# Kernel optimization log

Measured on AMD Instinct MI355X. Metric: run time of the kernel, lower is better.

## Reference

```python
import jax, jax.numpy as jnp
import numpy as np

B = 4096
DETER = 2048
BLOCKS = 8
HIDDEN = 256
SC, SD = 32, 16
STOCH = SC * SD  # 512
ACT = 17
EMBED = 1024
UNIMIX = 0.01
EPS = 1e-4
DPB = DETER // BLOCKS  # 256


def rmsnorm(x, scale):
    rms = jnp.sqrt(jnp.mean(x * x, axis=-1, keepdims=True) + EPS)
    return x / rms * scale


def dense(x, w, b):
    return x @ w + b


def block_linear(x, kernel, bias):
    # kernel: (out_per_block, in_per_block, blocks)
    bs = x.shape[:-1]
    ipb = x.shape[-1] // BLOCKS
    xg = x.reshape(*bs, BLOCKS, ipb)
    y = jnp.einsum('...gi,oig->...go', xg, kernel)
    return y.reshape(*bs, -1) + bias


def sample(logits):
    # unimix + straight-through argmax
    probs = jax.nn.softmax(logits, axis=-1)
    probs = (1.0 - UNIMIX) * probs + UNIMIX / SD
    logits = jnp.log(probs + 1e-8)
    soft = jax.nn.softmax(logits, axis=-1)
    hard = jax.nn.one_hot(jnp.argmax(logits, axis=-1), SD, dtype=soft.dtype)
    return hard + soft - jax.lax.stop_gradient(soft)


def setup_inputs() -> dict:
    key = jax.random.key(0)
    ks = jax.random.split(key, 16)

    def lecun(k, shape, fan_in):
        return jax.random.normal(k, shape, jnp.float32) / np.sqrt(fan_in)

    return {
        'stoch': jax.random.uniform(ks[0], (B, SC, SD), jnp.float32),
        'deter': jax.random.normal(ks[1], (B, DETER), jnp.float32),
        'action': jax.random.normal(ks[2], (B, ACT), jnp.float32),
        'embed': jax.random.normal(ks[3], (B, EMBED), jnp.float32),
        # Deter net params
        'in0_w': lecun(ks[4], (DETER, HIDDEN), DETER), 'in0_b': jnp.zeros((HIDDEN,)), 'in_norm0_s': jnp.ones((HIDDEN,)),
        'in1_w': lecun(ks[5], (STOCH, HIDDEN), STOCH), 'in1_b': jnp.zeros((HIDDEN,)), 'in_norm1_s': jnp.ones((HIDDEN,)),
        'in2_w': lecun(ks[6], (ACT, HIDDEN), ACT), 'in2_b': jnp.zeros((HIDDEN,)), 'in_norm2_s': jnp.ones((HIDDEN,)),
        'hid0_k': lecun(ks[7], (DPB, DPB + 3 * HIDDEN, BLOCKS), DPB + 3 * HIDDEN),
        'hid0_b': jnp.zeros((DETER,)), 'hid_norm0_s': jnp.ones((DETER,)),
        'gru_k': lecun(ks[8], (3 * DPB, DPB, BLOCKS), DPB), 'gru_b': jnp.zeros((3 * DETER,)),
        # posterior head
        'obs_fc0_w': lecun(ks[9], (DETER + EMBED, HIDDEN), DETER + EMBED), 'obs_fc0_b': jnp.zeros((HIDDEN,)),
        'obs_norm0_s': jnp.ones((HIDDEN,)),
        'obs_out_w': lecun(ks[10], (HIDDEN, STOCH), HIDDEN), 'obs_out_b': jnp.zeros((STOCH,)),
    }


def reference(stoch, deter, action, embed,
              in0_w, in0_b, in_norm0_s, in1_w, in1_b, in_norm1_s,
              in2_w, in2_b, in_norm2_s, hid0_k, hid0_b, hid_norm0_s,
              gru_k, gru_b, obs_fc0_w, obs_fc0_b, obs_norm0_s,
              obs_out_w, obs_out_b):
    Bn = stoch.shape[0]
    stoch_flat = stoch.reshape(Bn, -1)  # (B, 512)
    act = action / jnp.maximum(jnp.abs(action), 1.0)
    x0 = jax.nn.silu(rmsnorm(dense(deter, in0_w, in0_b), in_norm0_s))
    x1 = jax.nn.silu(rmsnorm(dense(stoch_flat, in1_w, in1_b), in_norm1_s))
    x2 = jax.nn.silu(rmsnorm(dense(act, in2_w, in2_b), in_norm2_s))
    x = jnp.concatenate([x0, x1, x2], axis=-1)  # (B, 768)
    x = jnp.broadcast_to(x[:, None, :], (Bn, BLOCKS, x.shape[-1]))
    deter_blocked = deter.reshape(Bn, BLOCKS, DPB)
    x = jnp.concatenate([deter_blocked, x], axis=-1).reshape(Bn, -1)  # (B, 8192)
    x = jax.nn.silu(rmsnorm(block_linear(x, hid0_k, hid0_b), hid_norm0_s))  # (B, 2048)
    gates = block_linear(x, gru_k, gru_b)  # (B, 6144)
    gates = gates.reshape(Bn, BLOCKS, 3 * DPB)
    g0, g1, g2 = jnp.split(gates, 3, axis=-1)
    reset = jax.nn.sigmoid(g0.reshape(Bn, -1))
    cand = g1.reshape(Bn, -1)
    update = jax.nn.sigmoid(g2.reshape(Bn, -1) - 1.0)
    new_deter = update * jnp.tanh(reset * cand) + (1.0 - update) * deter
    # posterior head
    h = jnp.concatenate([new_deter, embed], axis=-1)
    h = jax.nn.silu(rmsnorm(dense(h, obs_fc0_w, obs_fc0_b), obs_norm0_s))
    logit = dense(h, obs_out_w, obs_out_b).reshape(Bn, SC, SD)
    new_stoch = sample(logit)
    return (new_stoch, new_deter, logit)
```

## Files before the change

### kernel.cpp

```cpp
#include <hip/hip_runtime.h>
#include <cmath>

constexpr int BATCH = 4096;
constexpr float EPSN = 1e-4f;

constexpr int OFF_STOCH = 0;
constexpr int OFF_DETER = BATCH * 512;
constexpr int OFF_LOGIT = OFF_DETER + BATCH * 2048;

typedef unsigned short ushort;
typedef __attribute__((ext_vector_type(4))) float f32x4;
typedef __attribute__((ext_vector_type(8))) short s16x8;
struct us4 { ushort x, y, z, w; };

constexpr size_t U_WHH = 0;
constexpr size_t U_WHL = U_WHH + 2097152;
constexpr size_t U_WGH = U_WHL + 2097152;
constexpr size_t U_WGL = U_WGH + 1572864;
constexpr size_t U_WFH = U_WGL + 1572864;
constexpr size_t U_WFL = U_WFH + 786432;
constexpr size_t U_WOH = U_WFL + 786432;
constexpr size_t U_WOL = U_WOH + 131072;
constexpr size_t U_PEND = U_WOL + 131072;
constexpr size_t F_XB = U_PEND / 2;
constexpr size_t F_XH = F_XB + 3145728;
constexpr size_t U_X0H = (F_XH + 6291456) * 2;
constexpr size_t U_X0L = U_X0H + 524288;
constexpr size_t U_X1H = U_X0L + 524288;
constexpr size_t U_X1L = U_X1H + 131072;
constexpr size_t F_HB = F_XH + 4194304;

#define DINLINE __device__ __forceinline__

DINLINE float sigm(float x)  { return 1.0f / (1.0f + expf(-x)); }
DINLINE float siluf(float x) { return x / (1.0f + expf(-x)); }

DINLINE float4 ld4(const float* p) { return *reinterpret_cast<const float4*>(p); }
DINLINE void st4(float* p, float4 v) { *reinterpret_cast<float4*>(p) = v; }

DINLINE ushort f2bf(float x) {
  unsigned u = __float_as_uint(x);
  unsigned r = u + 0x7fffu + ((u >> 16) & 1u);
  return (ushort)(r >> 16);
}
DINLINE float bf2f(ushort h) { return __uint_as_float(((unsigned)h) << 16); }

DINLINE void cp16g(void* lds, const void* g) {
  __builtin_amdgcn_global_load_lds(
      (const __attribute__((address_space(1))) unsigned int*)g,
      (__attribute__((address_space(3))) unsigned int*)lds, 16, 0, 0);
}

DINLINE f32x4 mfma16(s16x8 a, s16x8 b, f32x4 c) {
  return __builtin_amdgcn_mfma_f32_16x16x32_bf16(a, b, c, 0, 0, 0);
}

DINLINE int swz_addr(int row, int kb0) {
  return (row * 64 + kb0) ^ ((row & 7) << 4);
}
DINLINE void dec_swz(int D, int& row, int& kb) {
  int r2 = (D >> 8) & 1;
  int r0 = ((D >> 6) & 1) ^ r2;
  row = ((D >> 7) << 1) | r0;
  kb = (D & 48) ^ ((row & 3) << 4);
}

DINLINE void split2(float x, ushort& h, ushort& l) {
  h = f2bf(x);
  l = f2bf(x - bf2f(h));
}

DINLINE size_t frag_idx(int n, int k, int NK) {
  return ((size_t)((n >> 4) * NK + (k >> 5)) * 64 + ((k >> 3) & 3) * 16 + (n & 15)) * 8 + (k & 7);
}

DINLINE float4 rms_silu4(float v0, float v1, float v2, float v3, float4 s4) {
  float ss = v0 * v0 + v1 * v1 + v2 * v2 + v3 * v3;
#pragma unroll
  for (int off = 32; off; off >>= 1) ss += __shfl_xor(ss, off);
  float inv = 1.0f / sqrtf(ss * (1.0f / 256.0f) + EPSN);
  float4 o;
  o.x = siluf(v0 * inv * s4.x); o.y = siluf(v1 * inv * s4.y);
  o.z = siluf(v2 * inv * s4.z); o.w = siluf(v3 * inv * s4.w);
  return o;
}

__global__ __launch_bounds__(256) void k_prep(
    const float* __restrict__ hk, const float* __restrict__ gk,
    const float* __restrict__ w0, const float* __restrict__ w1,
    const float* __restrict__ wf, const float* __restrict__ wo,
    ushort* __restrict__ wsU) {
  __shared__ float L[64 * 65];
  const int bid = blockIdx.x, tid = threadIdx.x;
  if (bid < 1792) {
    int t = bid * 256 + tid;
    if (t < 262144) {
      int o = t >> 10, i = t & 1023;
      const float* src = hk + (size_t)t * 8;
      float4 v0 = ld4(src), v1 = ld4(src + 4);
      float vv[8] = {v0.x, v0.y, v0.z, v0.w, v1.x, v1.y, v1.z, v1.w};
      size_t fi = frag_idx(o, i, 32);
#pragma unroll
      for (int g2 = 0; g2 < 8; ++g2) {
        ushort h, l; split2(vv[g2], h, l);
        wsU[U_WHH + (size_t)g2 * 262144 + fi] = h;
        wsU[U_WHL + (size_t)g2 * 262144 + fi] = l;
      }
    } else {
      int e = t - 262144;
      int o = e >> 8, i = e & 255;
      const float* src = gk + (size_t)e * 8;
      float4 v0 = ld4(src), v1 = ld4(src + 4);
      float vv[8] = {v0.x, v0.y, v0.z, v0.w, v1.x, v1.y, v1.z, v1.w};
      int gate = o >> 8, nc = (o >> 6) & 3, srow = gate * 64 + (o & 63);
      size_t fi = frag_idx(srow, i, 8);
#pragma unroll
      for (int g2 = 0; g2 < 8; ++g2) {
        ushort h, l; split2(vv[g2], h, l);
        size_t pb = (size_t)(g2 * 4 + nc) * 49152;
        wsU[U_WGH + pb + fi] = h;
        wsU[U_WGL + pb + fi] = l;
      }
    }
    return;
  }
  int t = bid - 1792;
  const float* src; ushort* dh; ushort* dl; int K, N;
  if (t < 128)      { src = w0; dh = wsU + U_X0H; dl = wsU + U_X0L; K = 2048; N = 256; }
  else if (t < 160) { t -= 128; src = w1; dh = wsU + U_X1H; dl = wsU + U_X1L; K = 512;  N = 256; }
  else if (t < 352) { t -= 160; src = wf; dh = wsU + U_WFH; dl = wsU + U_WFL; K = 3072; N = 256; }
  else              { t -= 352; src = wo; dh = wsU + U_WOH; dl = wsU + U_WOL; K = 256;  N = 512; }
  const int NK = K / 32;
  const int ntiles = N / 64;
  const int k0 = (t / ntiles) * 64, n0 = (t % ntiles) * 64;
#pragma unroll
  for (int q = 0; q < 4; ++q) {
    int row = q * 16 + (tid >> 4), col = (tid & 15) * 4;
    float4 v = ld4(src + (size_t)(k0 + row) * N + n0 + col);
    L[row * 65 + col]     = v.x;
    L[row * 65 + col + 1] = v.y;
    L[row * 65 + col + 2] = v.z;
    L[row * 65 + col + 3] = v.w;
  }
  __syncthreads();
  const int nl = tid >> 2, kc = (tid & 3) * 16;
  const int ng = n0 + nl;
  s16x8 h0, h1, l0v, l1v;
#pragma unroll
  for (int j = 0; j < 16; ++j) {
    ushort h, l; split2(L[(kc + j) * 65 + nl], h, l);
    if (j < 8) { h0[j] = (short)h; l0v[j] = (short)l; }
    else       { h1[j - 8] = (short)h; l1v[j - 8] = (short)l; }
  }
  size_t fa = frag_idx(ng, k0 + kc, NK);
  size_t fb = frag_idx(ng, k0 + kc + 8, NK);
  *(s16x8*)(dh + fa) = h0;
  *(s16x8*)(dh + fb) = h1;
  *(s16x8*)(dl + fa) = l0v;
  *(s16x8*)(dl + fb) = l1v;
}

__global__ __launch_bounds__(512) void k_gemm256(
    int mode,
    const float* __restrict__ deter, const float* __restrict__ stoch,
    const float* __restrict__ newdet, const float* __restrict__ embed,
    const ushort* __restrict__ wsU, float* __restrict__ part) {
  __shared__ ushort Ah[2][64 * 32], Al[2][64 * 32];
  const int tid = threadIdx.x, lane = tid & 63, wv = tid >> 6;
  const int wr = wv >> 2, wc = wv & 3;
  const int bid = blockIdx.x;
  constexpr size_t PL0 = (size_t)4096 * 512;

  const float* A0; const float* A1 = nullptr;
  int lda0, lda1 = 0, ksw = 1 << 30;
  const ushort* wFh; const ushort* wFl;
  int NKt, kch0, kbase, KT, m0, dstride, dcol;
  float* dst;

  if (mode == 0) {
    if (bid < 256) {
      int ks = bid & 3; m0 = (bid >> 2) * 64; kbase = ks * 512; KT = 16;
      A0 = deter; lda0 = 2048;
      wFh = wsU + U_X0H; wFl = wsU + U_X0L; NKt = 64; kch0 = ks * 16;
      dst = part + (size_t)(ks >> 1) * PL0; dstride = 512; dcol = (ks & 1) * 256;
    } else {
      int b = bid - 256; int ks = b & 1; m0 = (b >> 1) * 64; kbase = ks * 256; KT = 8;
      A0 = stoch; lda0 = 512;
      wFh = wsU + U_X1H; wFl = wsU + U_X1L; NKt = 16; kch0 = ks * 8;
      dst = part + 2 * PL0; dstride = 512; dcol = ks * 256;
    }
  } else {
    int ks = bid & 3; m0 = (bid >> 2) * 64; kbase = ks * 768; KT = 24;
    A0 = newdet; lda0 = 2048; A1 = embed; lda1 = 1024; ksw = 2048;
    wFh = wsU + U_WFH; wFl = wsU + U_WFL; NKt = 96; kch0 = ks * 24;
    dst = part + (size_t)ks * 4096 * 256; dstride = 256; dcol = 0;
  }

  const int arow = tid >> 2, akq = (tid & 3) * 8;
  const int abyte = swz_addr(arow, (tid & 3) * 16);
  float av[8];

  const f32x4 z4 = {0.f, 0.f, 0.f, 0.f};
  f32x4 acc[2][4];
#pragma unroll
  for (int i = 0; i < 2; ++i)
#pragma unroll
    for (int j = 0; j < 4; ++j) acc[i][j] = z4;

#define U_LOADA(kt) \
  if (tid < 256) { \
    int kg = kbase + (kt) * 32 + akq; \
    const float* p = (kg < ksw) ? A0 + (size_t)(m0 + arow) * lda0 + kg \
                                : A1 + (size_t)(m0 + arow) * lda1 + (kg - ksw); \
    float4 u_ = ld4(p), w_ = ld4(p + 4); \
    av[0] = u_.x; av[1] = u_.y; av[2] = u_.z; av[3] = u_.w; \
    av[4] = w_.x; av[5] = w_.y; av[6] = w_.z; av[7] = w_.w; \
  }
#define U_WRITEA(buf) \
  if (tid < 256) { \
    s16x8 h8, l8; \
    _Pragma("unroll") \
    for (int j = 0; j < 8; ++j) { \
      ushort h_, l_; split2(av[j], h_, l_); \
      h8[j] = (short)h_; l8[j] = (short)l_; \
    } \
    *(s16x8*)((char*)Ah[buf] + abyte) = h8; \
    *(s16x8*)((char*)Al[buf] + abyte) = l8; \
  }

  U_LOADA(0);
  U_WRITEA(0);
  __syncthreads();
  int cur = 0;
  for (int t = 0; t < KT; ++t) {
    if (t + 1 < KT) { U_LOADA(t + 1); }
    s16x8 bh[4], bl[4];
#pragma unroll
    for (int nf = 0; nf < 4; ++nf) {
      size_t fo = ((size_t)((wc * 4 + nf) * NKt + kch0 + t) * 64 + lane) * 8;
      bh[nf] = *(const s16x8*)(wFh + fo);
      bl[nf] = *(const s16x8*)(wFl + fo);
    }
    const int k16 = (lane >> 4) * 16;
    s16x8 afh[2], afl[2];
#pragma unroll
    for (int mf = 0; mf < 2; ++mf) {
      int by = swz_addr(wr * 32 + mf * 16 + (lane & 15), k16);
      afh[mf] = *(const s16x8*)((const char*)Ah[cur] + by);
      afl[mf] = *(const s16x8*)((const char*)Al[cur] + by);
    }
#pragma unroll
    for (int nf = 0; nf < 4; ++nf) {
#pragma unroll
      for (int mf = 0; mf < 2; ++mf) {
        acc[mf][nf] = mfma16(afh[mf], bh[nf], acc[mf][nf]);
        acc[mf][nf] = mfma16(afh[mf], bl[nf], acc[mf][nf]);
        acc[mf][nf] = mfma16(afl[mf], bh[nf], acc[mf][nf]);
      }
    }
    if (t + 1 < KT) { U_WRITEA(cur ^ 1); }
    __syncthreads();
    cur ^= 1;
  }
#undef U_LOADA
#undef U_WRITEA
#pragma unroll
  for (int mf = 0; mf < 2; ++mf) {
    int rbase = m0 + wr * 32 + mf * 16 + ((lane >> 4) << 2);
#pragma unroll
    for (int nf = 0; nf < 4; ++nf) {
      int col = dcol + wc * 64 + nf * 16 + (lane & 15);
#pragma unroll
      for (int r = 0; r < 4; ++r)
        dst[(size_t)(rbase + r) * dstride + col] = acc[mf][nf][r];
    }
  }
}

__global__ __launch_bounds__(512) void k_x2(
    const float* __restrict__ action, const float* __restrict__ w2,
    const float* __restrict__ b2, const float* __restrict__ s2,
    ushort* __restrict__ xbp) {
  __shared__ float W2s[17 * 256];
  __shared__ float A2s[128 * 20];
  const int tid = threadIdx.x, tx = tid & 63, wv = tid >> 6;
  const int m0 = blockIdx.x * 128;
  for (int e = tid; e < 17 * 256; e += 512) W2s[e] = w2[e];
  for (int e = tid; e < 128 * 17; e += 512) {
    int r = e / 17, c = e % 17;
    float a = action[(size_t)(m0 + r) * 17 + c];
    float m = fabsf(a);
    A2s[r * 20 + c] = a / (m > 1.f ? m : 1.f);
  }
  __syncthreads();
  float4 acc2[16];
#pragma unroll
  for (int r = 0; r < 16; ++r) acc2[r] = make_float4(0.f, 0.f, 0.f, 0.f);
#pragma unroll
  for (int k = 0; k < 17; ++k) {
    float4 w4 = ld4(W2s + k * 256 + tx * 4);
#pragma unroll
    for (int r = 0; r < 16; ++r) {
      float av = A2s[(wv * 16 + r) * 20 + k];
      acc2[r].x = fmaf(av, w4.x, acc2[r].x);
      acc2[r].y = fmaf(av, w4.y, acc2[r].y);
      acc2[r].z = fmaf(av, w4.z, acc2[r].z);
      acc2[r].w = fmaf(av, w4.w, acc2[r].w);
    }
  }
  float4 b4 = ld4(b2 + tx * 4);
  float4 s4 = ld4(s2 + tx * 4);
#pragma unroll
  for (int r = 0; r < 16; ++r) {
    float4 o = rms_silu4(acc2[r].x + b4.x, acc2[r].y + b4.y,
                         acc2[r].z + b4.z, acc2[r].w + b4.w, s4);
    us4 h4, l4;
    split2(o.x, h4.x, l4.x); split2(o.y, h4.y, l4.y);
    split2(o.z, h4.z, l4.z); split2(o.w, h4.w, l4.w);
    size_t rb = (size_t)(m0 + wv * 16 + r) * 1536;
    *(us4*)(xbp + rb + 512 + tx * 4) = h4;
    *(us4*)(xbp + rb + 768 + 512 + tx * 4) = l4;
  }
}

__global__ __launch_bounds__(256) void k_comb_in(
    const float* __restrict__ part,
    const float* __restrict__ b0, const float* __restrict__ s0,
    const float* __restrict__ b1, const float* __restrict__ s1,
    ushort* __restrict__ xbp) {
  const int tid = threadIdx.x, tx = tid & 63, wv = tid >> 6;
  const size_t row = blockIdx.x * 2 + (wv >> 1);
  const int half = wv & 1;
  constexpr size_t PL = (size_t)4096 * 512;
  float4 v = make_float4(0.f, 0.f, 0.f, 0.f);
  if (half == 0) {
#pragma unroll
    for (int p = 0; p < 2; ++p) {
      const float* s = part + p * PL + row * 512 + tx * 4;
      float4 a = ld4(s), b = ld4(s + 256);
      v.x += a.x + b.x; v.y += a.y + b.y; v.z += a.z + b.z; v.w += a.w + b.w;
    }
  } else {
    const float* s = part + 2 * PL + row * 512 + tx * 4;
    float4 a = ld4(s), b = ld4(s + 256);
    v.x = a.x + b.x; v.y = a.y + b.y; v.z = a.z + b.z; v.w = a.w + b.w;
  }
  const float* bp = half ? b1 : b0;
  const float* sp = half ? s1 : s0;
  float4 b4 = ld4(bp + tx * 4);
  float4 s4 = ld4(sp + tx * 4);
  float4 o = rms_silu4(v.x + b4.x, v.y + b4.y, v.z + b4.z, v.w + b4.w, s4);
  us4 h4, l4;
  split2(o.x, h4.x, l4.x); split2(o.y, h4.y, l4.y);
  split2(o.z, h4.z, l4.z); split2(o.w, h4.w, l4.w);
  *(us4*)(xbp + row * 1536 + half * 256 + tx * 4) = h4;
  *(us4*)(xbp + row * 1536 + 768 + half * 256 + tx * 4) = l4;
}

__global__ __launch_bounds__(256) void k_comb4(
    const float* __restrict__ part, const float* __restrict__ bias,
    const float* __restrict__ scale, ushort* __restrict__ hbp) {
  const int tid = threadIdx.x, tx = tid & 63, wv = tid >> 6;
  const size_t row = blockIdx.x * 4 + wv;
  float4 v = make_float4(0.f, 0.f, 0.f, 0.f);
#pragma unroll
  for (int ks = 0; ks < 4; ++ks) {
    float4 t = ld4(part + (size_t)ks * 4096 * 256 + row * 256 + tx * 4);
    v.x += t.x; v.y += t.y; v.z += t.z; v.w += t.w;
  }
  float4 b4 = ld4(bias + tx * 4);
  float4 s4 = ld4(scale + tx * 4);
  float4 o = rms_silu4(v.x + b4.x, v.y + b4.y, v.z + b4.z, v.w + b4.w, s4);
  us4 h4, l4;
  split2(o.x, h4.x, l4.x); split2(o.y, h4.y, l4.y);
  split2(o.z, h4.z, l4.z); split2(o.w, h4.w, l4.w);
  *(us4*)(hbp + row * 512 + tx * 4) = h4;
  *(us4*)(hbp + row * 512 + 256 + tx * 4) = l4;
}

__global__ __launch_bounds__(512) void k_hid0m(
    const float* __restrict__ deter, const ushort* __restrict__ xbp,
    const ushort* __restrict__ wsU,
    const float* __restrict__ hbias, float* __restrict__ yh) {
  __shared__ ushort Ah[2][64 * 32], Al[2][64 * 32];
  const int tid = threadIdx.x, lane = tid & 63, wv = tid >> 6;
  const int wr = wv >> 2, wc = wv & 3;
  const int g = blockIdx.x & 7;
  const int m0 = (int)(blockIdx.x >> 3) * 64;

  const ushort* whFh = wsU + U_WHH + (size_t)g * 262144;
  const ushort* whFl = wsU + U_WHL + (size_t)g * 262144;
  const char* xbB = (const char*)xbp;

  const int arow = tid >> 2, akq = (tid & 3) * 8;
  const int abyte = swz_addr(arow, (tid & 3) * 16);
  int an0, akb;
  dec_swz(tid * 16, an0, akb);
  float av[8];

  const f32x4 z4 = {0.f, 0.f, 0.f, 0.f};
  f32x4 acc[2][4];
#pragma unroll
  for (int i = 0; i < 2; ++i)
#pragma unroll
    for (int j = 0; j < 4; ++j) acc[i][j] = z4;

#define H_LOADA_DET(kt) \
  if (tid < 256) { \
    const float* p = deter + (size_t)(m0 + arow) * 2048 + g * 256 + (kt) * 32 + akq; \
    float4 u_ = ld4(p), w_ = ld4(p + 4); \
    av[0] = u_.x; av[1] = u_.y; av[2] = u_.z; av[3] = u_.w; \
    av[4] = w_.x; av[5] = w_.y; av[6] = w_.z; av[7] = w_.w; \
  }
#define H_WRITEA(buf) \
  if (tid < 256) { \
    s16x8 h8, l8; \
    _Pragma("unroll") \
    for (int j = 0; j < 8; ++j) { \
      ushort h_, l_; split2(av[j], h_, l_); \
      h8[j] = (short)h_; l8[j] = (short)l_; \
    } \
    *(s16x8*)((char*)Ah[buf] + abyte) = h8; \
    *(s16x8*)((char*)Al[buf] + abyte) = l8; \
  }
#define H_ISSUEA(buf, kt) \
  if (tid < 256) { \
    size_t rb = (size_t)(m0 + an0) * 3072; \
    int co = ((kt) * 32 - 256) * 2 + akb; \
    cp16g((char*)Ah[buf] + tid * 16, xbB + rb + co); \
    cp16g((char*)Al[buf] + tid * 16, xbB + rb + 1536 + co); \
  }

  H_LOADA_DET(0);
  H_WRITEA(0);
  __syncthreads();
  int cur = 0;
  for (int t = 0; t < 32; ++t) {
    const bool pf = (t + 1 < 32);
    const bool det = (t + 1 < 8);
    if (pf) {
      if (det) { H_LOADA_DET(t + 1); }
      else     { H_ISSUEA(cur ^ 1, t + 1); }
    }
    s16x8 bh[4], bl[4];
#pragma unroll
    for (int nf = 0; nf < 4; ++nf) {
      size_t fo = ((size_t)((wc * 4 + nf) * 32 + t) * 64 + lane) * 8;
      bh[nf] = *(const s16x8*)(whFh + fo);
      bl[nf] = *(const s16x8*)(whFl + fo);
    }
    const int k16 = (lane >> 4) * 16;
    s16x8 afh[2], afl[2];
#pragma unroll
    for (int mf = 0; mf < 2; ++mf) {
      int by = swz_addr(wr * 32 + mf * 16 + (lane & 15), k16);
      afh[mf] = *(const s16x8*)((const char*)Ah[cur] + by);
      afl[mf] = *(const s16x8*)((const char*)Al[cur] + by);
    }
#pragma unroll
    for (int nf = 0; nf < 4; ++nf) {
#pragma unroll
      for (int mf = 0; mf < 2; ++mf) {
        acc[mf][nf] = mfma16(afh[mf], bh[nf], acc[mf][nf]);
        acc[mf][nf] = mfma16(afh[mf], bl[nf], acc[mf][nf]);
        acc[mf][nf] = mfma16(afl[mf], bh[nf], acc[mf][nf]);
      }
    }
    if (pf && det) { H_WRITEA(cur ^ 1); }
    __syncthreads();
    cur ^= 1;
  }
#undef H_LOADA_DET
#undef H_WRITEA
#undef H_ISSUEA
#pragma unroll
  for (int mf = 0; mf < 2; ++mf) {
    int rbase = m0 + wr * 32 + mf * 16 + ((lane >> 4) << 2);
#pragma unroll
    for (int nf = 0; nf < 4; ++nf) {
      int col = wc * 64 + nf * 16 + (lane & 15);
      float b = hbias[g * 256 + col];
#pragma unroll
      for (int r = 0; r < 4; ++r)
        yh[(size_t)(rbase + r) * 2048 + g * 256 + col] = acc[mf][nf][r] + b;
    }
  }
}

__global__ __launch_bounds__(256) void k_rmsnorm2048(
    float* __restrict__ xh, const float* __restrict__ scale) {
  const int b = blockIdx.x, tid = threadIdx.x;
  float* row = xh + (size_t)b * 2048;
  float4 v0 = ld4(row + tid * 8);
  float4 v1 = ld4(row + tid * 8 + 4);
  float ss = v0.x * v0.x + v0.y * v0.y + v0.z * v0.z + v0.w * v0.w +
             v1.x * v1.x + v1.y * v1.y + v1.z * v1.z + v1.w * v1.w;
#pragma unroll
  for (int off = 32; off; off >>= 1) ss += __shfl_xor(ss, off);
  __shared__ float wsum[4];
  if ((tid & 63) == 0) wsum[tid >> 6] = ss;
  __syncthreads();
  float tot = wsum[0] + wsum[1] + wsum[2] + wsum[3];
  float inv = 1.0f / sqrtf(tot * (1.0f / 2048.0f) + EPSN);
  float4 sc0 = ld4(scale + tid * 8);
  float4 sc1 = ld4(scale + tid * 8 + 4);
  float o[8];
  o[0] = siluf(v0.x * inv * sc0.x); o[1] = siluf(v0.y * inv * sc0.y);
  o[2] = siluf(v0.z * inv * sc0.z); o[3] = siluf(v0.w * inv * sc0.w);
  o[4] = siluf(v1.x * inv * sc1.x); o[5] = siluf(v1.y * inv * sc1.y);
  o[6] = siluf(v1.z * inv * sc1.z); o[7] = siluf(v1.w * inv * sc1.w);
  s16x8 h8, l8;
#pragma unroll
  for (int j = 0; j < 8; ++j) {
    ushort h, l; split2(o[j], h, l);
    h8[j] = (short)h; l8[j] = (short)l;
  }
  ushort* rp = (ushort*)row;
  *(s16x8*)(rp + tid * 8) = h8;
  *(s16x8*)(rp + 2048 + tid * 8) = l8;
}

__global__ __launch_bounds__(512) void k_grum(
    const ushort* __restrict__ xhp, const ushort* __restrict__ wsU,
    const float* __restrict__ gb, const float* __restrict__ deter,
    float* __restrict__ newdet) {
  __shared__ ushort Ah[2][128 * 32], Al[2][128 * 32];
  const int tid = threadIdx.x, lane = tid & 63, wv = tid >> 6;
  const int wr = wv >> 2, wc = wv & 3;
  const int g = blockIdx.x & 7;
  const int nc = (int)(blockIdx.x >> 3) & 3;
  const int m0 = (int)(blockIdx.x >> 5) * 128;

  const ushort* wgFh = wsU + U_WGH + (size_t)(g * 4 + nc) * 49152;
  const ushort* wgFl = wsU + U_WGL + (size_t)(g * 4 + nc) * 49152;

  const char* xhB = (const char*)xhp;
  int an0, akb;
  dec_swz(tid * 16, an0, akb);

  const f32x4 z4 = {0.f, 0.f, 0.f, 0.f};
  f32x4 acc[4][3];
#pragma unroll
  for (int i = 0; i < 4; ++i)
#pragma unroll
    for (int j = 0; j < 3; ++j) acc[i][j] = z4;

#define G_ISSUEA(buf, kt) { \
    size_t rb = (size_t)(m0 + an0) * 8192; \
    int co = (g * 256 + (kt) * 32) * 2 + akb; \
    cp16g((char*)Ah[buf] + tid * 16, xhB + rb + co); \
    cp16g((char*)Al[buf] + tid * 16, xhB + rb + 4096 + co); \
  }

  G_ISSUEA(0, 0);
  __syncthreads();
  int cur = 0;
  for (int t = 0; t < 8; ++t) {
    if (t + 1 < 8) { G_ISSUEA(cur ^ 1, t + 1); }
    s16x8 bh[3], bl[3];
#pragma unroll
    for (int gt = 0; gt < 3; ++gt) {
      size_t fo = ((size_t)((gt * 4 + wc) * 8 + t) * 64 + lane) * 8;
      bh[gt] = *(const s16x8*)(wgFh + fo);
      bl[gt] = *(const s16x8*)(wgFl + fo);
    }
    const int k16 = (lane >> 4) * 16;
    s16x8 afh[4], afl[4];
#pragma unroll
    for (int mf = 0; mf < 4; ++mf) {
      int by = swz_addr(wr * 64 + mf * 16 + (lane & 15), k16);
      afh[mf] = *(const s16x8*)((const char*)Ah[cur] + by);
      afl[mf] = *(const s16x8*)((const char*)Al[cur] + by);
    }
#pragma unroll
    for (int gt = 0; gt < 3; ++gt) {
#pragma unroll
      for (int mf = 0; mf < 4; ++mf) {
        acc[mf][gt] = mfma16(afh[mf], bh[gt], acc[mf][gt]);
        acc[mf][gt] = mfma16(afh[mf], bl[gt], acc[mf][gt]);
        acc[mf][gt] = mfma16(afl[mf], bh[gt], acc[mf][gt]);
      }
    }
    __syncthreads();
    cur ^= 1;
  }
#undef G_ISSUEA
  const int col = nc * 64 + wc * 16 + (lane & 15);
  const float br = gb[g * 768 + col];
  const float bc = gb[g * 768 + 256 + col];
  const float bu = gb[g * 768 + 512 + col];
#pragma unroll
  for (int mf = 0; mf < 4; ++mf) {
    int rbase = m0 + wr * 64 + mf * 16 + ((lane >> 4) << 2);
#pragma unroll
    for (int r = 0; r < 4; ++r) {
      int row = rbase + r;
      float rr = sigm(acc[mf][0][r] + br);
      float cc = acc[mf][1][r] + bc;
      float uu = sigm(acc[mf][2][r] + bu - 1.0f);
      float d = deter[(size_t)row * 2048 + g * 256 + col];
      newdet[(size_t)row * 2048 + g * 256 + col] =
          uu * tanhf(rr * cc) + (1.0f - uu) * d;
    }
  }
}

__global__ __launch_bounds__(512) void k_obsoutm(
    const ushort* __restrict__ hbp, const ushort* __restrict__ wsU,
    const float* __restrict__ ob, float* __restrict__ logit) {
  __shared__ ushort Ah[2][64 * 32], Al[2][64 * 32];
  const int tid = threadIdx.x, lane = tid & 63, wv = tid >> 6;
  const int wr = wv >> 2, wc = wv & 3;
  const int half = blockIdx.x & 1;
  const int m0 = (int)(blockIdx.x >> 1) * 64;

  const ushort* woFh = wsU + U_WOH;
  const ushort* woFl = wsU + U_WOL;
  const char* hbB = (const char*)hbp;
  int an0, akb;
  dec_swz(tid * 16, an0, akb);

  const f32x4 z4 = {0.f, 0.f, 0.f, 0.f};
  f32x4 acc[2][4];
#pragma unroll
  for (int i = 0; i < 2; ++i)
#pragma unroll
    for (int j = 0; j < 4; ++j) acc[i][j] = z4;

#define O_ISSUEA(buf, kt) \
  if (tid < 256) { \
    size_t rb = (size_t)(m0 + an0) * 1024; \
    int co = (kt) * 64 + akb; \
    cp16g((char*)Ah[buf] + tid * 16, hbB + rb + co); \
    cp16g((char*)Al[buf] + tid * 16, hbB + rb + 512 + co); \
  }

  O_ISSUEA(0, 0);
  __syncthreads();
  int cur = 0;
  for (int t = 0; t < 8; ++t) {
    if (t + 1 < 8) { O_ISSUEA(cur ^ 1, t + 1); }
    s16x8 bh[4], bl[4];
#pragma unroll
    for (int nf = 0; nf < 4; ++nf) {
      size_t fo = ((size_t)((half * 16 + wc * 4 + nf) * 8 + t) * 64 + lane) * 8;
      bh[nf] = *(const s16x8*)(woFh + fo);
      bl[nf] = *(const s16x8*)(woFl + fo);
    }
    const int k16 = (lane >> 4) * 16;
    s16x8 afh[2], afl[2];
#pragma unroll
    for (int mf = 0; mf < 2; ++mf) {
      int by = swz_addr(wr * 32 + mf * 16 + (lane & 15), k16);
      afh[mf] = *(const s16x8*)((const char*)Ah[cur] + by);
      afl[mf] = *(const s16x8*)((const char*)Al[cur] + by);
    }
#pragma unroll
    for (int nf = 0; nf < 4; ++nf) {
#pragma unroll
      for (int mf = 0; mf < 2; ++mf) {
        acc[mf][nf] = mfma16(afh[mf], bh[nf], acc[mf][nf]);
        acc[mf][nf] = mfma16(afh[mf], bl[nf], acc[mf][nf]);
        acc[mf][nf] = mfma16(afl[mf], bh[nf], acc[mf][nf]);
      }
    }
    __syncthreads();
    cur ^= 1;
  }
#undef O_ISSUEA
#pragma unroll
  for (int mf = 0; mf < 2; ++mf) {
    int rbase = m0 + wr * 32 + mf * 16 + ((lane >> 4) << 2);
#pragma unroll
    for (int nf = 0; nf < 4; ++nf) {
      int col = half * 256 + wc * 64 + nf * 16 + (lane & 15);
      float b = ob[col];
#pragma unroll
      for (int r = 0; r < 4; ++r)
        logit[(size_t)(rbase + r) * 512 + col] = acc[mf][nf][r] + b;
    }
  }
}

__global__ __launch_bounds__(256) void k_argmax(
    const float* __restrict__ logit, float* __restrict__ stoch_out) {
  const size_t row = blockIdx.x * 4 + (threadIdx.x >> 6);
  const int lane = threadIdx.x & 63;
  const float* lp = logit + row * 512 + lane * 8;
  float4 a = ld4(lp), b = ld4(lp + 4);
  float v[8] = {a.x, a.y, a.z, a.w, b.x, b.y, b.z, b.w};
  float bv = v[0]; int bi = 0;
#pragma unroll
  for (int j = 1; j < 8; ++j)
    if (v[j] > bv) { bv = v[j]; bi = j; }
  bi += lane * 8;
  float pv = __shfl_xor(bv, 1);
  int   pi = __shfl_xor(bi, 1);
  if (pv > bv || (pv == bv && pi < bi)) { bv = pv; bi = pi; }
  float4 o0, o1;
  int base = lane * 8;
  o0.x = (bi == base + 0) ? 1.f : 0.f;
  o0.y = (bi == base + 1) ? 1.f : 0.f;
  o0.z = (bi == base + 2) ? 1.f : 0.f;
  o0.w = (bi == base + 3) ? 1.f : 0.f;
  o1.x = (bi == base + 4) ? 1.f : 0.f;
  o1.y = (bi == base + 5) ? 1.f : 0.f;
  o1.z = (bi == base + 6) ? 1.f : 0.f;
  o1.w = (bi == base + 7) ? 1.f : 0.f;
  st4(stoch_out + row * 512 + base, o0);
  st4(stoch_out + row * 512 + base + 4, o1);
}

extern "C" void kernel_launch(void* const* d_in, const int* in_sizes, int n_in,
                              void* d_out, int out_size, void* d_ws, size_t ws_size,
                              hipStream_t stream) {
  (void)in_sizes; (void)n_in; (void)out_size; (void)ws_size;
  const float* stoch      = (const float*)d_in[0];
  const float* deter      = (const float*)d_in[1];
  const float* action     = (const float*)d_in[2];
  const float* embed      = (const float*)d_in[3];
  const float* in0_w      = (const float*)d_in[4];
  const float* in0_b      = (const float*)d_in[5];
  const float* n0_s       = (const float*)d_in[6];
  const float* in1_w      = (const float*)d_in[7];
  const float* in1_b      = (const float*)d_in[8];
  const float* n1_s       = (const float*)d_in[9];
  const float* in2_w      = (const float*)d_in[10];
  const float* in2_b      = (const float*)d_in[11];
  const float* n2_s       = (const float*)d_in[12];
  const float* hid0_k     = (const float*)d_in[13];
  const float* hid0_b     = (const float*)d_in[14];
  const float* hidn_s     = (const float*)d_in[15];
  const float* gru_k      = (const float*)d_in[16];
  const float* gru_b      = (const float*)d_in[17];
  const float* obs_fc0_w  = (const float*)d_in[18];
  const float* obs_fc0_b  = (const float*)d_in[19];
  const float* obs_n_s    = (const float*)d_in[20];
  const float* obs_out_w  = (const float*)d_in[21];
  const float* obs_out_b  = (const float*)d_in[22];

  float*  out = (float*)d_out;
  float*  ws  = (float*)d_ws;
  ushort* wsU = (ushort*)d_ws;
  ushort* xbp = (ushort*)(ws + F_XB);
  float*  xh  = ws + F_XH;
  ushort* xhp = (ushort*)(ws + F_XH);
  ushort* hbp = (ushort*)(ws + F_HB);
  float*  part = xh;

  hipLaunchKernelGGL(k_prep, dim3(2176), dim3(256), 0, stream,
                     hid0_k, gru_k, in0_w, in1_w, obs_fc0_w, obs_out_w, wsU);
  hipLaunchKernelGGL(k_x2, dim3(32), dim3(512), 0, stream,
                     action, in2_w, in2_b, n2_s, xbp);
  hipLaunchKernelGGL(k_gemm256, dim3(384), dim3(512), 0, stream,
                     0, deter, stoch, out + OFF_DETER, embed, wsU, part);
  hipLaunchKernelGGL(k_comb_in, dim3(2048), dim3(256), 0, stream,
                     part, in0_b, n0_s, in1_b, n1_s, xbp);
  hipLaunchKernelGGL(k_hid0m, dim3(512), dim3(512), 0, stream,
                     deter, xbp, wsU, hid0_b, xh);
  hipLaunchKernelGGL(k_rmsnorm2048, dim3(4096), dim3(256), 0, stream, xh, hidn_s);
  hipLaunchKernelGGL(k_grum, dim3(1024), dim3(512), 0, stream,
                     xhp, wsU, gru_b, deter, out + OFF_DETER);
  hipLaunchKernelGGL(k_gemm256, dim3(256), dim3(512), 0, stream,
                     1, deter, stoch, out + OFF_DETER, embed, wsU, part);
  hipLaunchKernelGGL(k_comb4, dim3(1024), dim3(256), 0, stream,
                     part, obs_fc0_b, obs_n_s, hbp);
  hipLaunchKernelGGL(k_obsoutm, dim3(128), dim3(512), 0, stream,
                     hbp, wsU, obs_out_b, out + OFF_LOGIT);
  hipLaunchKernelGGL(k_argmax, dim3(1024), dim3(256), 0, stream,
                     out + OFF_LOGIT, out + OFF_STOCH);
}
```

Measured before the change: 258.1 us.

## Prefetch B weight fragments one k-step ahead in MFMA GEMMs; widen k_x2 grid

In all four MFMA GEMM kernels, the per-iteration global loads of the B (weight) fragments are moved out of the loop head into a register prefetch. The next step's fragments are issued after the current step's MFMAs, so their latency overlaps the barrier and the next iteration's work instead of stalling the MFMAs. Separately, k_x2 is relaunched with 256 blocks of 256 threads handling 16 rows each instead of 32 blocks of 128 rows, to spread this small kernel over more CUs. The register prefetch raises VGPR pressure, which may reduce occupancy.

```diff
diff --git a/kernel.cpp b/kernel.cpp
--- a/kernel.cpp
+++ b/kernel.cpp
@@ -199,6 +199,7 @@
   const int arow = tid >> 2, akq = (tid & 3) * 8;
   const int abyte = swz_addr(arow, (tid & 3) * 16);
   float av[8];
+  s16x8 bh[4], bl[4];
 
   const f32x4 z4 = {0.f, 0.f, 0.f, 0.f};
   f32x4 acc[2][4];
@@ -227,20 +228,21 @@
     *(s16x8*)((char*)Ah[buf] + abyte) = h8; \
     *(s16x8*)((char*)Al[buf] + abyte) = l8; \
   }
+#define U_LOADB(kt) { \
+    _Pragma("unroll") \
+    for (int nf = 0; nf < 4; ++nf) { \
+      size_t fo = ((size_t)((wc * 4 + nf) * NKt + kch0 + (kt)) * 64 + lane) * 8; \
+      bh[nf] = *(const s16x8*)(wFh + fo); \
+      bl[nf] = *(const s16x8*)(wFl + fo); \
+    } }
 
   U_LOADA(0);
   U_WRITEA(0);
+  U_LOADB(0);
   __syncthreads();
   int cur = 0;
   for (int t = 0; t < KT; ++t) {
     if (t + 1 < KT) { U_LOADA(t + 1); }
-    s16x8 bh[4], bl[4];
-#pragma unroll
-    for (int nf = 0; nf < 4; ++nf) {
-      size_t fo = ((size_t)((wc * 4 + nf) * NKt + kch0 + t) * 64 + lane) * 8;
-      bh[nf] = *(const s16x8*)(wFh + fo);
-      bl[nf] = *(const s16x8*)(wFl + fo);
-    }
     const int k16 = (lane >> 4) * 16;
     s16x8 afh[2], afl[2];
 #pragma unroll
@@ -258,12 +260,13 @@
         acc[mf][nf] = mfma16(afl[mf], bh[nf], acc[mf][nf]);
       }
     }
-    if (t + 1 < KT) { U_WRITEA(cur ^ 1); }
+    if (t + 1 < KT) { U_LOADB(t + 1); U_WRITEA(cur ^ 1); }
     __syncthreads();
     cur ^= 1;
   }
 #undef U_LOADA
 #undef U_WRITEA
+#undef U_LOADB
 #pragma unroll
   for (int mf = 0; mf < 2; ++mf) {
     int rbase = m0 + wr * 32 + mf * 16 + ((lane >> 4) << 2);
@@ -277,31 +280,31 @@
   }
 }
 
-__global__ __launch_bounds__(512) void k_x2(
+__global__ __launch_bounds__(256) void k_x2(
     const float* __restrict__ action, const float* __restrict__ w2,
     const float* __restrict__ b2, const float* __restrict__ s2,
     ushort* __restrict__ xbp) {
   __shared__ float W2s[17 * 256];
-  __shared__ float A2s[128 * 20];
+  __shared__ float A2s[16 * 20];
   const int tid = threadIdx.x, tx = tid & 63, wv = tid >> 6;
-  const int m0 = blockIdx.x * 128;
-  for (int e = tid; e < 17 * 256; e += 512) W2s[e] = w2[e];
-  for (int e = tid; e < 128 * 17; e += 512) {
+  const int m0 = blockIdx.x * 16;
+  for (int e = tid; e < 17 * 256; e += 256) W2s[e] = w2[e];
+  for (int e = tid; e < 272; e += 256) {
     int r = e / 17, c = e % 17;
     float a = action[(size_t)(m0 + r) * 17 + c];
     float m = fabsf(a);
     A2s[r * 20 + c] = a / (m > 1.f ? m : 1.f);
   }
   __syncthreads();
-  float4 acc2[16];
-#pragma unroll
-  for (int r = 0; r < 16; ++r) acc2[r] = make_float4(0.f, 0.f, 0.f, 0.f);
+  float4 acc2[4];
+#pragma unroll
+  for (int r = 0; r < 4; ++r) acc2[r] = make_float4(0.f, 0.f, 0.f, 0.f);
 #pragma unroll
   for (int k = 0; k < 17; ++k) {
     float4 w4 = ld4(W2s + k * 256 + tx * 4);
 #pragma unroll
-    for (int r = 0; r < 16; ++r) {
-      float av = A2s[(wv * 16 + r) * 20 + k];
+    for (int r = 0; r < 4; ++r) {
+      float av = A2s[(wv * 4 + r) * 20 + k];
       acc2[r].x = fmaf(av, w4.x, acc2[r].x);
       acc2[r].y = fmaf(av, w4.y, acc2[r].y);
       acc2[r].z = fmaf(av, w4.z, acc2[r].z);
@@ -311,13 +314,13 @@
   float4 b4 = ld4(b2 + tx * 4);
   float4 s4 = ld4(s2 + tx * 4);
 #pragma unroll
-  for (int r = 0; r < 16; ++r) {
+  for (int r = 0; r < 4; ++r) {
     float4 o = rms_silu4(acc2[r].x + b4.x, acc2[r].y + b4.y,
                          acc2[r].z + b4.z, acc2[r].w + b4.w, s4);
     us4 h4, l4;
     split2(o.x, h4.x, l4.x); split2(o.y, h4.y, l4.y);
     split2(o.z, h4.z, l4.z); split2(o.w, h4.w, l4.w);
-    size_t rb = (size_t)(m0 + wv * 16 + r) * 1536;
+    size_t rb = (size_t)(m0 + wv * 4 + r) * 1536;
     *(us4*)(xbp + rb + 512 + tx * 4) = h4;
     *(us4*)(xbp + rb + 768 + 512 + tx * 4) = l4;
   }
@@ -397,6 +400,7 @@
   int an0, akb;
   dec_swz(tid * 16, an0, akb);
   float av[8];
+  s16x8 bh[4], bl[4];
 
   const f32x4 z4 = {0.f, 0.f, 0.f, 0.f};
   f32x4 acc[2][4];
@@ -430,9 +434,17 @@
     cp16g((char*)Ah[buf] + tid * 16, xbB + rb + co); \
     cp16g((char*)Al[buf] + tid * 16, xbB + rb + 1536 + co); \
   }
+#define H_LOADB(kt) { \
+    _Pragma("unroll") \
+    for (int nf = 0; nf < 4; ++nf) { \
+      size_t fo = ((size_t)((wc * 4 + nf) * 32 + (kt)) * 64 + lane) * 8; \
+      bh[nf] = *(const s16x8*)(whFh + fo); \
+      bl[nf] = *(const s16x8*)(whFl + fo); \
+    } }
 
   H_LOADA_DET(0);
   H_WRITEA(0);
+  H_LOADB(0);
   __syncthreads();
   int cur = 0;
   for (int t = 0; t < 32; ++t) {
@@ -442,13 +454,6 @@
       if (det) { H_LOADA_DET(t + 1); }
       else     { H_ISSUEA(cur ^ 1, t + 1); }
     }
-    s16x8 bh[4], bl[4];
-#pragma unroll
-    for (int nf = 0; nf < 4; ++nf) {
-      size_t fo = ((size_t)((wc * 4 + nf) * 32 + t) * 64 + lane) * 8;
-      bh[nf] = *(const s16x8*)(whFh + fo);
-      bl[nf] = *(const s16x8*)(whFl + fo);
-    }
     const int k16 = (lane >> 4) * 16;
     s16x8 afh[2], afl[2];
 #pragma unroll
@@ -466,6 +471,7 @@
         acc[mf][nf] = mfma16(afl[mf], bh[nf], acc[mf][nf]);
       }
     }
+    if (pf) { H_LOADB(t + 1); }
     if (pf && det) { H_WRITEA(cur ^ 1); }
     __syncthreads();
     cur ^= 1;
@@ -473,6 +479,7 @@
 #undef H_LOADA_DET
 #undef H_WRITEA
 #undef H_ISSUEA
+#undef H_LOADB
 #pragma unroll
   for (int mf = 0; mf < 2; ++mf) {
     int rbase = m0 + wr * 32 + mf * 16 + ((lane >> 4) << 2);
@@ -537,6 +544,7 @@
   const char* xhB = (const char*)xhp;
   int an0, akb;
   dec_swz(tid * 16, an0, akb);
+  s16x8 bh[3], bl[3];
 
   const f32x4 z4 = {0.f, 0.f, 0.f, 0.f};
   f32x4 acc[4][3];
@@ -551,19 +559,20 @@
     cp16g((char*)Ah[buf] + tid * 16, xhB + rb + co); \
     cp16g((char*)Al[buf] + tid * 16, xhB + rb + 4096 + co); \
   }
+#define G_LOADB(kt) { \
+    _Pragma("unroll") \
+    for (int gt = 0; gt < 3; ++gt) { \
+      size_t fo = ((size_t)((gt * 4 + wc) * 8 + (kt)) * 64 + lane) * 8; \
+      bh[gt] = *(const s16x8*)(wgFh + fo); \
+      bl[gt] = *(const s16x8*)(wgFl + fo); \
+    } }
 
   G_ISSUEA(0, 0);
+  G_LOADB(0);
   __syncthreads();
   int cur = 0;
   for (int t = 0; t < 8; ++t) {
     if (t + 1 < 8) { G_ISSUEA(cur ^ 1, t + 1); }
-    s16x8 bh[3], bl[3];
-#pragma unroll
-    for (int gt = 0; gt < 3; ++gt) {
-      size_t fo = ((size_t)((gt * 4 + wc) * 8 + t) * 64 + lane) * 8;
-      bh[gt] = *(const s16x8*)(wgFh + fo);
-      bl[gt] = *(const s16x8*)(wgFl + fo);
-    }
     const int k16 = (lane >> 4) * 16;
     s16x8 afh[4], afl[4];
 #pragma unroll
@@ -581,10 +590,12 @@
         acc[mf][gt] = mfma16(afl[mf], bh[gt], acc[mf][gt]);
       }
     }
+    if (t + 1 < 8) { G_LOADB(t + 1); }
     __syncthreads();
     cur ^= 1;
   }
 #undef G_ISSUEA
+#undef G_LOADB
   const int col = nc * 64 + wc * 16 + (lane & 15);
   const float br = gb[g * 768 + col];
   const float bc = gb[g * 768 + 256 + col];
@@ -619,6 +630,7 @@
   const char* hbB = (const char*)hbp;
   int an0, akb;
   dec_swz(tid * 16, an0, akb);
+  s16x8 bh[4], bl[4];
 
   const f32x4 z4 = {0.f, 0.f, 0.f, 0.f};
   f32x4 acc[2][4];
@@ -634,19 +646,20 @@
     cp16g((char*)Ah[buf] + tid * 16, hbB + rb + co); \
     cp16g((char*)Al[buf] + tid * 16, hbB + rb + 512 + co); \
   }
+#define O_LOADB(kt) { \
+    _Pragma("unroll") \
+    for (int nf = 0; nf < 4; ++nf) { \
+      size_t fo = ((size_t)((half * 16 + wc * 4 + nf) * 8 + (kt)) * 64 + lane) * 8; \
+      bh[nf] = *(const s16x8*)(woFh + fo); \
+      bl[nf] = *(const s16x8*)(woFl + fo); \
+    } }
 
   O_ISSUEA(0, 0);
+  O_LOADB(0);
   __syncthreads();
   int cur = 0;
   for (int t = 0; t < 8; ++t) {
     if (t + 1 < 8) { O_ISSUEA(cur ^ 1, t + 1); }
-    s16x8 bh[4], bl[4];
-#pragma unroll
-    for (int nf = 0; nf < 4; ++nf) {
-      size_t fo = ((size_t)((half * 16 + wc * 4 + nf) * 8 + t) * 64 + lane) * 8;
-      bh[nf] = *(const s16x8*)(woFh + fo);
-      bl[nf] = *(const s16x8*)(woFl + fo);
-    }
     const int k16 = (lane >> 4) * 16;
     s16x8 afh[2], afl[2];
 #pragma unroll
@@ -664,10 +677,12 @@
         acc[mf][nf] = mfma16(afl[mf], bh[nf], acc[mf][nf]);
       }
     }
+    if (t + 1 < 8) { O_LOADB(t + 1); }
     __syncthreads();
     cur ^= 1;
   }
 #undef O_ISSUEA
+#undef O_LOADB
 #pragma unroll
   for (int mf = 0; mf < 2; ++mf) {
     int rbase = m0 + wr * 32 + mf * 16 + ((lane >> 4) << 2);
@@ -750,7 +765,7 @@
 
   hipLaunchKernelGGL(k_prep, dim3(2176), dim3(256), 0, stream,
                      hid0_k, gru_k, in0_w, in1_w, obs_fc0_w, obs_out_w, wsU);
-  hipLaunchKernelGGL(k_x2, dim3(32), dim3(512), 0, stream,
+  hipLaunchKernelGGL(k_x2, dim3(256), dim3(256), 0, stream,
                      action, in2_w, in2_b, n2_s, xbp);
   hipLaunchKernelGGL(k_gemm256, dim3(384), dim3(512), 0, stream,
                      0, deter, stoch, out + OFF_DETER, embed, wsU, part);
```

New measurement: 218.1 us. 15.5% less time.

## Split k_x2 and k_grum into smaller tiles and preload full A tile in GRU

Applied to the files above, without the earlier changes.

k_x2 now runs 256 blocks of 256 threads, each handling 16 rows instead of 128, to spread the tiny action projection across more CUs. k_grum halves the M tile to 64 rows and doubles the grid to 2048 blocks. It also replaces the double-buffered per-k-step A loads with a single upfront load of the whole 64x256 hi/lo A tile into shared memory (64 KB), followed by one barrier and a sync-free MFMA loop. The intent is more parallelism and less barrier overhead, at the cost of losing load/compute overlap, more weight re-reads per row, and higher LDS use per block that may limit occupancy.

```diff
diff --git a/kernel.cpp b/kernel.cpp
--- a/kernel.cpp
+++ b/kernel.cpp
@@ -277,31 +277,31 @@
   }
 }
 
-__global__ __launch_bounds__(512) void k_x2(
+__global__ __launch_bounds__(256) void k_x2(
     const float* __restrict__ action, const float* __restrict__ w2,
     const float* __restrict__ b2, const float* __restrict__ s2,
     ushort* __restrict__ xbp) {
   __shared__ float W2s[17 * 256];
-  __shared__ float A2s[128 * 20];
+  __shared__ float A2s[16 * 20];
   const int tid = threadIdx.x, tx = tid & 63, wv = tid >> 6;
-  const int m0 = blockIdx.x * 128;
-  for (int e = tid; e < 17 * 256; e += 512) W2s[e] = w2[e];
-  for (int e = tid; e < 128 * 17; e += 512) {
+  const int m0 = blockIdx.x * 16;
+  for (int e = tid; e < 17 * 256; e += 256) W2s[e] = w2[e];
+  for (int e = tid; e < 272; e += 256) {
     int r = e / 17, c = e % 17;
     float a = action[(size_t)(m0 + r) * 17 + c];
     float m = fabsf(a);
     A2s[r * 20 + c] = a / (m > 1.f ? m : 1.f);
   }
   __syncthreads();
-  float4 acc2[16];
-#pragma unroll
-  for (int r = 0; r < 16; ++r) acc2[r] = make_float4(0.f, 0.f, 0.f, 0.f);
+  float4 acc2[4];
+#pragma unroll
+  for (int r = 0; r < 4; ++r) acc2[r] = make_float4(0.f, 0.f, 0.f, 0.f);
 #pragma unroll
   for (int k = 0; k < 17; ++k) {
     float4 w4 = ld4(W2s + k * 256 + tx * 4);
 #pragma unroll
-    for (int r = 0; r < 16; ++r) {
-      float av = A2s[(wv * 16 + r) * 20 + k];
+    for (int r = 0; r < 4; ++r) {
+      float av = A2s[(wv * 4 + r) * 20 + k];
       acc2[r].x = fmaf(av, w4.x, acc2[r].x);
       acc2[r].y = fmaf(av, w4.y, acc2[r].y);
       acc2[r].z = fmaf(av, w4.z, acc2[r].z);
@@ -311,13 +311,13 @@
   float4 b4 = ld4(b2 + tx * 4);
   float4 s4 = ld4(s2 + tx * 4);
 #pragma unroll
-  for (int r = 0; r < 16; ++r) {
+  for (int r = 0; r < 4; ++r) {
     float4 o = rms_silu4(acc2[r].x + b4.x, acc2[r].y + b4.y,
                          acc2[r].z + b4.z, acc2[r].w + b4.w, s4);
     us4 h4, l4;
     split2(o.x, h4.x, l4.x); split2(o.y, h4.y, l4.y);
     split2(o.z, h4.z, l4.z); split2(o.w, h4.w, l4.w);
-    size_t rb = (size_t)(m0 + wv * 16 + r) * 1536;
+    size_t rb = (size_t)(m0 + wv * 4 + r) * 1536;
     *(us4*)(xbp + rb + 512 + tx * 4) = h4;
     *(us4*)(xbp + rb + 768 + 512 + tx * 4) = l4;
   }
@@ -524,39 +524,39 @@
     const ushort* __restrict__ xhp, const ushort* __restrict__ wsU,
     const float* __restrict__ gb, const float* __restrict__ deter,
     float* __restrict__ newdet) {
-  __shared__ ushort Ah[2][128 * 32], Al[2][128 * 32];
+  __shared__ ushort Ah[8][64 * 32], Al[8][64 * 32];
   const int tid = threadIdx.x, lane = tid & 63, wv = tid >> 6;
   const int wr = wv >> 2, wc = wv & 3;
   const int g = blockIdx.x & 7;
   const int nc = (int)(blockIdx.x >> 3) & 3;
-  const int m0 = (int)(blockIdx.x >> 5) * 128;
+  const int m0 = (int)(blockIdx.x >> 5) * 64;
 
   const ushort* wgFh = wsU + U_WGH + (size_t)(g * 4 + nc) * 49152;
   const ushort* wgFl = wsU + U_WGL + (size_t)(g * 4 + nc) * 49152;
-
   const char* xhB = (const char*)xhp;
-  int an0, akb;
-  dec_swz(tid * 16, an0, akb);
+
+#pragma unroll
+  for (int q = 0; q < 4; ++q) {
+    int lin = q * 8192 + tid * 16;
+    int chunk = lin >> 12;
+    int within = lin & 4095;
+    int row, kb;
+    dec_swz(within, row, kb);
+    size_t src = (size_t)(m0 + row) * 8192 + (size_t)(g * 256 + chunk * 32) * 2 + kb;
+    cp16g((char*)Ah + lin, xhB + src);
+    cp16g((char*)Al + lin, xhB + src + 4096);
+  }
+  __syncthreads();
 
   const f32x4 z4 = {0.f, 0.f, 0.f, 0.f};
-  f32x4 acc[4][3];
-#pragma unroll
-  for (int i = 0; i < 4; ++i)
+  f32x4 acc[2][3];
+#pragma unroll
+  for (int i = 0; i < 2; ++i)
 #pragma unroll
     for (int j = 0; j < 3; ++j) acc[i][j] = z4;
 
-#define G_ISSUEA(buf, kt) { \
-    size_t rb = (size_t)(m0 + an0) * 8192; \
-    int co = (g * 256 + (kt) * 32) * 2 + akb; \
-    cp16g((char*)Ah[buf] + tid * 16, xhB + rb + co); \
-    cp16g((char*)Al[buf] + tid * 16, xhB + rb + 4096 + co); \
-  }
-
-  G_ISSUEA(0, 0);
-  __syncthreads();
-  int cur = 0;
+#pragma unroll
   for (int t = 0; t < 8; ++t) {
-    if (t + 1 < 8) { G_ISSUEA(cur ^ 1, t + 1); }
     s16x8 bh[3], bl[3];
 #pragma unroll
     for (int gt = 0; gt < 3; ++gt) {
@@ -565,33 +565,30 @@
       bl[gt] = *(const s16x8*)(wgFl + fo);
     }
     const int k16 = (lane >> 4) * 16;
-    s16x8 afh[4], afl[4];
-#pragma unroll
-    for (int mf = 0; mf < 4; ++mf) {
-      int by = swz_addr(wr * 64 + mf * 16 + (lane & 15), k16);
-      afh[mf] = *(const s16x8*)((const char*)Ah[cur] + by);
-      afl[mf] = *(const s16x8*)((const char*)Al[cur] + by);
+    s16x8 afh[2], afl[2];
+#pragma unroll
+    for (int mf = 0; mf < 2; ++mf) {
+      int by = swz_addr(wr * 32 + mf * 16 + (lane & 15), k16);
+      afh[mf] = *(const s16x8*)((const char*)Ah[t] + by);
+      afl[mf] = *(const s16x8*)((const char*)Al[t] + by);
     }
 #pragma unroll
     for (int gt = 0; gt < 3; ++gt) {
 #pragma unroll
-      for (int mf = 0; mf < 4; ++mf) {
+      for (int mf = 0; mf < 2; ++mf) {
         acc[mf][gt] = mfma16(afh[mf], bh[gt], acc[mf][gt]);
         acc[mf][gt] = mfma16(afh[mf], bl[gt], acc[mf][gt]);
         acc[mf][gt] = mfma16(afl[mf], bh[gt], acc[mf][gt]);
       }
     }
-    __syncthreads();
-    cur ^= 1;
-  }
-#undef G_ISSUEA
+  }
   const int col = nc * 64 + wc * 16 + (lane & 15);
   const float br = gb[g * 768 + col];
   const float bc = gb[g * 768 + 256 + col];
   const float bu = gb[g * 768 + 512 + col];
 #pragma unroll
-  for (int mf = 0; mf < 4; ++mf) {
-    int rbase = m0 + wr * 64 + mf * 16 + ((lane >> 4) << 2);
+  for (int mf = 0; mf < 2; ++mf) {
+    int rbase = m0 + wr * 32 + mf * 16 + ((lane >> 4) << 2);
 #pragma unroll
     for (int r = 0; r < 4; ++r) {
       int row = rbase + r;
@@ -750,7 +747,7 @@
 
   hipLaunchKernelGGL(k_prep, dim3(2176), dim3(256), 0, stream,
                      hid0_k, gru_k, in0_w, in1_w, obs_fc0_w, obs_out_w, wsU);
-  hipLaunchKernelGGL(k_x2, dim3(32), dim3(512), 0, stream,
+  hipLaunchKernelGGL(k_x2, dim3(256), dim3(256), 0, stream,
                      action, in2_w, in2_b, n2_s, xbp);
   hipLaunchKernelGGL(k_gemm256, dim3(384), dim3(512), 0, stream,
                      0, deter, stoch, out + OFF_DETER, embed, wsU, part);
@@ -759,7 +756,7 @@
   hipLaunchKernelGGL(k_hid0m, dim3(512), dim3(512), 0, stream,
                      deter, xbp, wsU, hid0_b, xh);
   hipLaunchKernelGGL(k_rmsnorm2048, dim3(4096), dim3(256), 0, stream, xh, hidn_s);
-  hipLaunchKernelGGL(k_grum, dim3(1024), dim3(512), 0, stream,
+  hipLaunchKernelGGL(k_grum, dim3(2048), dim3(512), 0, stream,
                      xhp, wsU, gru_b, deter, out + OFF_DETER);
   hipLaunchKernelGGL(k_gemm256, dim3(256), dim3(512), 0, stream,
                      1, deter, stoch, out + OFF_DETER, embed, wsU, part);
```

After: 250.2 us. 3.1% less time.
